# Performance work log

Measured on AMD Instinct MI355X. Metric: run time of the kernel, lower is better.

## Reference

```python
import jax, jax.numpy as jnp
import numpy as np

DT = 0.01          # Euler step size
ALPHA = 1.0        # Grubb exponent (hardcoded in forward())
V0 = 0.02          # resting venous blood volume fraction
NOISE_AMP = 0.01   # amplitude of per-step noise injected into the neural drive
T = 1000           # integration length (hardcoded in forward())
B = 16384          # batch of independent simulations


def setup_inputs() -> dict:
    key = jax.random.key(0)
    noise = jax.random.normal(key, (T, B), dtype=jnp.float32)
    f32 = lambda v: jnp.asarray(v, dtype=jnp.float32)
    return {
        "noise": noise,
        "sigma": f32(0.9),
        "mu": f32(0.8),
        "lamb": f32(0.3),
        "beta": f32(0.9),
        "psi": f32(0.5),
        "phi": f32(2.0),
        "chi": f32(0.3),
    }


def reference(noise, sigma, mu, lamb, beta, psi, phi, chi):
    # Balloon-Windkessel BOLD model, explicit Euler, per-step noise.
    # States per simulation: s (vasodilatory signal), f (flow), v (volume), q (dHb).
    b = noise.shape[1]
    inv_alpha = 1.0 / ALPHA

    def step(carry, z):
        s, f, v, q = carry
        # oxygen extraction fraction E(f) = 1 - (1 - E0)^(1/f)
        E = 1.0 - (1.0 - beta) ** (1.0 / f)
        v_a = v ** inv_alpha  # outflow v^(1/alpha)
        s2 = s + DT * (NOISE_AMP * z - sigma * s - mu * (f - 1.0))
        f2 = f + DT * s
        v2 = v + DT * (f - v_a) / lamb
        q2 = q + DT * (f * E / beta - v_a * q / v) / lamb
        # BOLD readout at the new state
        y = V0 * (phi * (1.0 - q2) + psi * (1.0 - q2 / v2) + chi * (1.0 - v2))
        return (s2, f2, v2, q2), y

    init = (
        jnp.zeros((b,), noise.dtype),
        jnp.ones((b,), noise.dtype),
        jnp.ones((b,), noise.dtype),
        jnp.ones((b,), noise.dtype),
    )
    _, ys = jax.lax.scan(step, init, noise)  # ys: [T, B]
    return ys
```

## Files before the change

### kernel.cpp

```cpp
#include <hip/hip_runtime.h>


#define BATCH    16384
#define ROW2     (BATCH / 2)
#define DT       0.01f
#define NOISE_AMP 0.01f
#define V0       0.02f
#define CHUNKS   40
#define CL       25
#define LPR      16
#define NTHREADS (CHUNKS * LPR)
#define SCAND    6

typedef float v2f __attribute__((ext_vector_type(2)));

#if __has_builtin(__builtin_amdgcn_exp2f)
#define EXP2F(x) __builtin_amdgcn_exp2f(x)
#else
#define EXP2F(x) exp2f(x)
#endif

__device__ __forceinline__ float uf(float x) {
    return __uint_as_float(__builtin_amdgcn_readfirstlane(__float_as_uint(x)));
}

struct D22 { double a, b, c, d; };
__device__ __forceinline__ D22 dmul(D22 x, D22 y) {
    D22 r;
    r.a = x.a * y.a + x.b * y.c;  r.b = x.a * y.b + x.b * y.d;
    r.c = x.c * y.a + x.d * y.c;  r.d = x.c * y.b + x.d * y.d;
    return r;
}

__global__ __launch_bounds__(NTHREADS, 5) void balloon_scan(
    const float* __restrict__ noise,
    const float* __restrict__ p_sigma,
    const float* __restrict__ p_mu,
    const float* __restrict__ p_lamb,
    const float* __restrict__ p_beta,
    const float* __restrict__ p_psi,
    const float* __restrict__ p_phi,
    const float* __restrict__ p_chi,
    float* __restrict__ out)
{
    const int tid  = threadIdx.x;
    const int lane = tid & (LPR - 1);
    const int cc   = tid >> 4;

    const float sigma = uf(p_sigma[0]);
    const float mu    = uf(p_mu[0]);
    const float lamb  = uf(p_lamb[0]);
    const float beta  = uf(p_beta[0]);
    const float psi   = uf(p_psi[0]);
    const float phi   = uf(p_phi[0]);
    const float chi   = uf(p_chi[0]);

    const float as_   = 1.0f - DT * sigma;
    const float dtn   = DT * NOISE_AMP;
    const float dtm   = DT * mu;
    const float dt_il = uf((float)(0.01 / (double)lamb));
    const float av    = 1.0f - dt_il;
    const float kq    = uf(dt_il / beta);
    const float lc    = uf(log2f(1.0f - beta));
    const float c0 = V0 * (phi + psi + chi), c1 = V0 * phi, c2 = V0 * psi, c3 = V0 * chi;

    D22 A; A.a = 1.0 - 0.01 * (double)sigma; A.b = -0.01 * (double)mu;
           A.c = 0.01;                       A.d = 1.0;
    D22 A2 = dmul(A, A), A4 = dmul(A2, A2), A8 = dmul(A4, A4), A16 = dmul(A8, A8);
    D22 P  = dmul(dmul(A16, A8), A);
    double avd = 1.0 - 0.01 / (double)lamb;
    double av2 = avd * avd, av4 = av2 * av2, av8 = av4 * av4, av16 = av8 * av8;
    double ap  = av16 * av8 * avd;

    float M11[SCAND], M12[SCAND], M21[SCAND], M22[SCAND], AVP[SCAND];
#pragma unroll
    for (int j = 0; j < SCAND; ++j) {
        M11[j] = uf((float)P.a); M12[j] = uf((float)P.b);
        M21[j] = uf((float)P.c); M22[j] = uf((float)P.d);
        AVP[j] = uf((float)ap);
        P = dmul(P, P); ap = ap * ap;
    }

    float ws = 0.0f, wf = 1.0f, avc = 1.0f;
#pragma unroll
    for (int j = 0; j < SCAND; ++j) {
        if ((cc >> j) & 1) {
            const float t = __builtin_fmaf(M11[j], ws, M12[j] * wf);
            wf = __builtin_fmaf(M21[j], ws, M22[j] * wf);
            ws = t; avc *= AVP[j];
        }
    }

    auto sfstep = [&](float& s, float& f, float zz) {
        const float s2 = __builtin_fmaf(as_, s,
                         __builtin_fmaf(dtn, zz,
                         __builtin_fmaf(-dtm, f, dtm)));
        f = __builtin_fmaf(DT, s, f);
        s = s2;
    };
    auto vqfwd = [&](float f_, float& accv, float& accq) {
        const float invf = __builtin_amdgcn_rcpf(f_);
        const float e2   = EXP2F(lc * invf);
        const float t1   = __builtin_fmaf(-f_, e2, f_);
        accv = __builtin_fmaf(av, accv, dt_il * f_);
        accq = __builtin_fmaf(av, accq, kq * t1);
    };

    __shared__ float4 ssc[NTHREADS];

    const v2f* zg = (const v2f*)noise + (cc * CL) * ROW2 + blockIdx.x * LPR + lane;
    v2f z[CL];

    float rs0 = 0.f, rf0 = 0.f, rs1 = 0.f, rf1 = 0.f;
#pragma unroll
    for (int j = 0; j < CL; ++j) {
        z[j] = zg[j * ROW2];
        sfstep(rs0, rf0, z[j].x);
        sfstep(rs1, rf1, z[j].y);
    }

    ssc[tid] = make_float4(rs0, rf0, rs1, rf1);
    __syncthreads();
#pragma unroll
    for (int j = 0; j < SCAND; ++j) {
        const int off = 1 << j;
        const bool has = (cc >= off);
        float4 n = make_float4(0.f, 0.f, 0.f, 0.f);
        if (has) n = ssc[tid - off * LPR];
        __syncthreads();
        if (has) {
            rs0 = __builtin_fmaf(M11[j], n.x, __builtin_fmaf(M12[j], n.y, rs0));
            rf0 = __builtin_fmaf(M21[j], n.x, __builtin_fmaf(M22[j], n.y, rf0));
            rs1 = __builtin_fmaf(M11[j], n.z, __builtin_fmaf(M12[j], n.w, rs1));
            rf1 = __builtin_fmaf(M21[j], n.z, __builtin_fmaf(M22[j], n.w, rf1));
            ssc[tid] = make_float4(rs0, rf0, rs1, rf1);
        }
        __syncthreads();
    }
    float s0a = ws, f0a = wf, s0b = ws, f0b = wf;
    if (cc > 0) {
        const float4 pr = ssc[tid - LPR];
        s0a += pr.x; f0a += pr.y; s0b += pr.z; f0b += pr.w;
    }
    __syncthreads();

    float sa = s0a, fa = f0a, sb = s0b, fb = f0b;
    float Rv0 = 0.f, Rq0 = 0.f, Rv1 = 0.f, Rq1 = 0.f;
#pragma unroll
    for (int j = 0; j < CL; ++j) {
        vqfwd(fa, Rv0, Rq0);
        vqfwd(fb, Rv1, Rq1);
        sfstep(sa, fa, z[j].x);
        sfstep(sb, fb, z[j].y);
    }

    ssc[tid] = make_float4(Rv0, Rq0, Rv1, Rq1);
    __syncthreads();
#pragma unroll
    for (int j = 0; j < SCAND; ++j) {
        const int off = 1 << j;
        const bool has = (cc >= off);
        float4 n = make_float4(0.f, 0.f, 0.f, 0.f);
        if (has) n = ssc[tid - off * LPR];
        __syncthreads();
        if (has) {
            Rv0 = __builtin_fmaf(AVP[j], n.x, Rv0);
            Rq0 = __builtin_fmaf(AVP[j], n.y, Rq0);
            Rv1 = __builtin_fmaf(AVP[j], n.z, Rv1);
            Rq1 = __builtin_fmaf(AVP[j], n.w, Rq1);
            ssc[tid] = make_float4(Rv0, Rq0, Rv1, Rq1);
        }
        __syncthreads();
    }
    float va = avc, qa = avc, vb = avc, qb = avc;
    if (cc > 0) {
        const float4 pr = ssc[tid - LPR];
        va += pr.x; qa += pr.y; vb += pr.z; qb += pr.w;
    }

    sa = s0a; fa = f0a; sb = s0b; fb = f0b;
    v2f* og = (v2f*)out + (cc * CL) * ROW2 + blockIdx.x * LPR + lane;
#pragma unroll
    for (int j = 0; j < CL; ++j) {
        vqfwd(fa, va, qa);
        vqfwd(fb, vb, qb);
        sfstep(sa, fa, z[j].x);
        sfstep(sb, fb, z[j].y);

        const float ia = __builtin_amdgcn_rcpf(va);
        const float ib = __builtin_amdgcn_rcpf(vb);
        v2f y2;
        y2.x = __builtin_fmaf(-c2, qa * ia,
               __builtin_fmaf(-c3, va,
               __builtin_fmaf(-c1, qa, c0)));
        y2.y = __builtin_fmaf(-c2, qb * ib,
               __builtin_fmaf(-c3, vb,
               __builtin_fmaf(-c1, qb, c0)));
        __builtin_nontemporal_store(y2, og + j * ROW2);
    }
}

extern "C" void kernel_launch(void* const* d_in, const int* in_sizes, int n_in,
                              void* d_out, int out_size, void* d_ws, size_t ws_size,
                              hipStream_t stream) {
    const float* noise   = (const float*)d_in[0];
    const float* p_sigma = (const float*)d_in[1];
    const float* p_mu    = (const float*)d_in[2];
    const float* p_lamb  = (const float*)d_in[3];
    const float* p_beta  = (const float*)d_in[4];
    const float* p_psi   = (const float*)d_in[5];
    const float* p_phi   = (const float*)d_in[6];
    const float* p_chi   = (const float*)d_in[7];

    balloon_scan<<<BATCH / (2 * LPR), NTHREADS, 0, stream>>>(
        noise, p_sigma, p_mu, p_lamb, p_beta, p_psi, p_phi, p_chi,
        (float*)d_out);
}
```

Measured before the change: 159.9 us.

## Process one simulation per thread and cache flow values instead of recomputing s/f

```diff
diff --git a/kernel.cpp b/kernel.cpp
--- a/kernel.cpp
+++ b/kernel.cpp
@@ -2,7 +2,6 @@
 
 
 #define BATCH    16384
-#define ROW2     (BATCH / 2)
 #define DT       0.01f
 #define NOISE_AMP 0.01f
 #define V0       0.02f
@@ -12,8 +11,6 @@
 #define NTHREADS (CHUNKS * LPR)
 #define SCAND    6
 
-typedef float v2f __attribute__((ext_vector_type(2)));
-
 #if __has_builtin(__builtin_amdgcn_exp2f)
 #define EXP2F(x) __builtin_amdgcn_exp2f(x)
 #else
@@ -32,7 +29,7 @@
     return r;
 }
 
-__global__ __launch_bounds__(NTHREADS, 5) void balloon_scan(
+__global__ __launch_bounds__(NTHREADS, 6) void balloon_scan(
     const float* __restrict__ noise,
     const float* __restrict__ p_sigma,
     const float* __restrict__ p_mu,
@@ -46,6 +43,7 @@
     const int tid  = threadIdx.x;
     const int lane = tid & (LPR - 1);
     const int cc   = tid >> 4;
+    const int sim  = blockIdx.x * LPR + lane;
 
     const float sigma = uf(p_sigma[0]);
     const float mu    = uf(p_mu[0]);
@@ -106,97 +104,82 @@
         accq = __builtin_fmaf(av, accq, kq * t1);
     };
 
-    __shared__ float4 ssc[NTHREADS];
-
-    const v2f* zg = (const v2f*)noise + (cc * CL) * ROW2 + blockIdx.x * LPR + lane;
-    v2f z[CL];
-
-    float rs0 = 0.f, rf0 = 0.f, rs1 = 0.f, rf1 = 0.f;
+    __shared__ float2 ss[NTHREADS];
+
+    const float* zp = noise + (cc * CL) * BATCH + sim;
+    float z[CL];
+
+    float rs = 0.f, rf = 0.f;
 #pragma unroll
     for (int j = 0; j < CL; ++j) {
-        z[j] = zg[j * ROW2];
-        sfstep(rs0, rf0, z[j].x);
-        sfstep(rs1, rf1, z[j].y);
-    }
-
-    ssc[tid] = make_float4(rs0, rf0, rs1, rf1);
+        z[j] = zp[j * BATCH];
+        sfstep(rs, rf, z[j]);
+    }
+
+    ss[tid] = make_float2(rs, rf);
     __syncthreads();
 #pragma unroll
     for (int j = 0; j < SCAND; ++j) {
         const int off = 1 << j;
         const bool has = (cc >= off);
-        float4 n = make_float4(0.f, 0.f, 0.f, 0.f);
-        if (has) n = ssc[tid - off * LPR];
+        float2 n = make_float2(0.f, 0.f);
+        if (has) n = ss[tid - off * LPR];
         __syncthreads();
         if (has) {
-            rs0 = __builtin_fmaf(M11[j], n.x, __builtin_fmaf(M12[j], n.y, rs0));
-            rf0 = __builtin_fmaf(M21[j], n.x, __builtin_fmaf(M22[j], n.y, rf0));
-            rs1 = __builtin_fmaf(M11[j], n.z, __builtin_fmaf(M12[j], n.w, rs1));
-            rf1 = __builtin_fmaf(M21[j], n.z, __builtin_fmaf(M22[j], n.w, rf1));
-            ssc[tid] = make_float4(rs0, rf0, rs1, rf1);
+            rs = __builtin_fmaf(M11[j], n.x, __builtin_fmaf(M12[j], n.y, rs));
+            rf = __builtin_fmaf(M21[j], n.x, __builtin_fmaf(M22[j], n.y, rf));
+            ss[tid] = make_float2(rs, rf);
         }
         __syncthreads();
     }
-    float s0a = ws, f0a = wf, s0b = ws, f0b = wf;
+    float s = ws, f = wf;
     if (cc > 0) {
-        const float4 pr = ssc[tid - LPR];
-        s0a += pr.x; f0a += pr.y; s0b += pr.z; f0b += pr.w;
+        const float2 pr = ss[tid - LPR];
+        s += pr.x; f += pr.y;
     }
     __syncthreads();
 
-    float sa = s0a, fa = f0a, sb = s0b, fb = f0b;
-    float Rv0 = 0.f, Rq0 = 0.f, Rv1 = 0.f, Rq1 = 0.f;
+    float Rv = 0.f, Rq = 0.f;
 #pragma unroll
     for (int j = 0; j < CL; ++j) {
-        vqfwd(fa, Rv0, Rq0);
-        vqfwd(fb, Rv1, Rq1);
-        sfstep(sa, fa, z[j].x);
-        sfstep(sb, fb, z[j].y);
-    }
-
-    ssc[tid] = make_float4(Rv0, Rq0, Rv1, Rq1);
+        const float zz = z[j];
+        z[j] = f;
+        vqfwd(f, Rv, Rq);
+        sfstep(s, f, zz);
+    }
+
+    ss[tid] = make_float2(Rv, Rq);
     __syncthreads();
 #pragma unroll
     for (int j = 0; j < SCAND; ++j) {
         const int off = 1 << j;
         const bool has = (cc >= off);
-        float4 n = make_float4(0.f, 0.f, 0.f, 0.f);
-        if (has) n = ssc[tid - off * LPR];
+        float2 n = make_float2(0.f, 0.f);
+        if (has) n = ss[tid - off * LPR];
         __syncthreads();
         if (has) {
-            Rv0 = __builtin_fmaf(AVP[j], n.x, Rv0);
-            Rq0 = __builtin_fmaf(AVP[j], n.y, Rq0);
-            Rv1 = __builtin_fmaf(AVP[j], n.z, Rv1);
-            Rq1 = __builtin_fmaf(AVP[j], n.w, Rq1);
-            ssc[tid] = make_float4(Rv0, Rq0, Rv1, Rq1);
+            Rv = __builtin_fmaf(AVP[j], n.x, Rv);
+            Rq = __builtin_fmaf(AVP[j], n.y, Rq);
+            ss[tid] = make_float2(Rv, Rq);
         }
         __syncthreads();
     }
-    float va = avc, qa = avc, vb = avc, qb = avc;
+    float v = avc, q = avc;
     if (cc > 0) {
-        const float4 pr = ssc[tid - LPR];
-        va += pr.x; qa += pr.y; vb += pr.z; qb += pr.w;
-    }
-
-    sa = s0a; fa = f0a; sb = s0b; fb = f0b;
-    v2f* og = (v2f*)out + (cc * CL) * ROW2 + blockIdx.x * LPR + lane;
+        const float2 pr = ss[tid - LPR];
+        v += pr.x; q += pr.y;
+    }
+
+    float* op = out + (cc * CL) * BATCH + sim;
 #pragma unroll
     for (int j = 0; j < CL; ++j) {
-        vqfwd(fa, va, qa);
-        vqfwd(fb, vb, qb);
-        sfstep(sa, fa, z[j].x);
-        sfstep(sb, fb, z[j].y);
-
-        const float ia = __builtin_amdgcn_rcpf(va);
-        const float ib = __builtin_amdgcn_rcpf(vb);
-        v2f y2;
-        y2.x = __builtin_fmaf(-c2, qa * ia,
-               __builtin_fmaf(-c3, va,
-               __builtin_fmaf(-c1, qa, c0)));
-        y2.y = __builtin_fmaf(-c2, qb * ib,
-               __builtin_fmaf(-c3, vb,
-               __builtin_fmaf(-c1, qb, c0)));
-        __builtin_nontemporal_store(y2, og + j * ROW2);
+        const float fj = z[j];
+        vqfwd(fj, v, q);
+        const float iv = __builtin_amdgcn_rcpf(v);
+        const float y = __builtin_fmaf(-c2, q * iv,
+                        __builtin_fmaf(-c3, v,
+                        __builtin_fmaf(-c1, q, c0)));
+        __builtin_nontemporal_store(y, op + j * BATCH);
     }
 }
 
@@ -212,7 +195,7 @@
     const float* p_phi   = (const float*)d_in[6];
     const float* p_chi   = (const float*)d_in[7];
 
-    balloon_scan<<<BATCH / (2 * LPR), NTHREADS, 0, stream>>>(
+    balloon_scan<<<BATCH / LPR, NTHREADS, 0, stream>>>(
         noise, p_sigma, p_mu, p_lamb, p_beta, p_psi, p_phi, p_chi,
         (float*)d_out);
 }
```

Result: faster. 154.7 us (-3.3%).
